# Kernel optimization log

Hardware: AMD Instinct MI355X
Metric: run time of the kernel (lower is better)

## Reference

```python
import jax, jax.numpy as jnp
import numpy as np

CLASH_WEIGHT = 0.05
PHYSICS_WEIGHT = 0.3
CLAMP_DIST = 10.0
EPS = 1e-8
C_IDX, N_IDX = 0, 1  # ATOM_TYPE_MAP['C'], ATOM_TYPE_MAP['N']


def setup_inputs() -> dict:
    key = jax.random.key(0)
    ks = jax.random.split(key, 8)
    B, R, A = 2, 1024, 4096
    return {
        'rots_pred': jax.random.normal(ks[0], (B, R, 3, 3), dtype=jnp.float32),
        'trans_pred': jax.random.normal(ks[1], (B, R, 3), dtype=jnp.float32),
        'coords_pred': jax.random.normal(ks[2], (B, A, 3), dtype=jnp.float32),
        'rots_true': jax.random.normal(ks[3], (B, R, 3, 3), dtype=jnp.float32),
        'trans_true': jax.random.normal(ks[4], (B, R, 3), dtype=jnp.float32),
        'coords_true': jax.random.normal(ks[5], (B, A, 3), dtype=jnp.float32),
        'atom_types': jax.random.randint(ks[6], (B, A), 0, 19, dtype=jnp.int32),
        'vdw_radii': jax.random.uniform(ks[7], (19,), dtype=jnp.float32),
        'res_mask': jnp.ones((B, R), dtype=jnp.float32),
        'mask': jnp.ones((B, A), dtype=jnp.float32),
    }


def _local_coords(rots, trans, coords):
    # invert_frames: R^-1 = R^T, t^-1 = -R^T t ; apply to all points per frame
    inv_rots = jnp.swapaxes(rots, -1, -2)                      # [B,R,3,3]
    inv_trans = -jnp.einsum('brij,brj->bri', inv_rots, trans)  # [B,R,3]
    # [B, R, A, 3]
    return jnp.einsum('brij,baj->brai', inv_rots, coords) + inv_trans[:, :, None, :]


def _pairwise_dist(coords, eps2=1e-12):
    # numerically-stable cdist via squared-norm expansion
    sq = jnp.sum(coords * coords, axis=-1)                      # [B,A]
    d2 = sq[:, :, None] + sq[:, None, :] - 2.0 * jnp.einsum('bad,bcd->bac', coords, coords)
    return jnp.sqrt(jnp.maximum(d2, eps2))                      # [B,A,A]


def reference(rots_pred, trans_pred, coords_pred, rots_true, trans_true,
              coords_true, atom_types, vdw_radii, res_mask, mask):
    # ---- FAPE ----
    lp = _local_coords(rots_pred, trans_pred, coords_pred)   # [B,R,A,3]
    lt = _local_coords(rots_true, trans_true, coords_true)   # [B,R,A,3]
    err = jnp.sqrt(jnp.sum((lp - lt) ** 2, axis=-1) + EPS)   # [B,R,A]
    err = jnp.minimum(err, CLAMP_DIST)
    err = err * mask[:, None, :] * res_mask[:, :, None]
    fape = jnp.sum(err) / (jnp.sum(mask) * jnp.sum(res_mask) + EPS)

    # shared pairwise distances on predicted coords
    d = _pairwise_dist(coords_pred)                          # [B,A,A]

    # ---- Clash ----
    radii = vdw_radii[atom_types]                            # [B,A]
    min_d = radii[:, :, None] + radii[:, None, :]
    clashes = (d < min_d) & (d > EPS)
    num_clashes = jnp.sum(clashes.astype(jnp.float32), axis=(-1, -2)) / 2.0
    num_atoms = coords_pred.shape[-2]
    clash = jnp.mean(num_clashes / num_atoms)

    # ---- Physics (C-N peptide bond length) ----
    is_c = atom_types == C_IDX
    is_n = atom_types == N_IDX
    cn_mask = (is_c[:, :, None] & is_n[:, None, :]).astype(jnp.float32)
    penalty = jax.nn.relu(jnp.abs(d - 1.33) - 0.2) * cn_mask
    total_pen = jnp.sum(penalty, axis=(-1, -2))
    n_pairs = jnp.maximum(jnp.sum(cn_mask, axis=(-1, -2)), 1.0)
    physics = jnp.mean(total_pen / n_pairs)

    total = fape + CLASH_WEIGHT * clash + PHYSICS_WEIGHT * physics
    return total
```

## Files before the change

kernel.cpp:

```cpp
#include <hip/hip_runtime.h>


constexpr int BB = 2;
constexpr int FR = 4;
constexpr int NI = 4;
constexpr int TJ = 16;
constexpr int IC = 1024;

constexpr int NB_FAPE = 512;
constexpr int NB_BAND = 512;
constexpr int NB_FULL = 768;
constexpr int NB_PAIR = NB_BAND + NB_FULL;

__device__ __forceinline__ float wred(float v) {
#pragma unroll
  for (int o = 32; o > 0; o >>= 1) v += __shfl_down(v, o, 64);
  return v;
}
__device__ __forceinline__ double wredd(double v) {
#pragma unroll
  for (int o = 32; o > 0; o >>= 1) v += __shfl_down(v, o, 64);
  return v;
}

template <bool BAND>
__device__ __forceinline__ void pair_body(
    const float* __restrict__ coords, const int* __restrict__ types,
    const float* __restrict__ vdw, int A, int b, int ic, int jt, int tid,
    float& out_clash, float& out_pen) {
  const int ibase = ic * IC;
  float xi[NI], yi[NI], zi[NI], qi[NI], ri[NI], cf[NI], nf[NI];
  int ii[NI];
#pragma unroll
  for (int k = 0; k < NI; ++k) {
    ii[k] = ibase + (k << 8) + tid;
    const size_t g = (size_t)b * A + ii[k];
    const float x = coords[g * 3], y = coords[g * 3 + 1], z = coords[g * 3 + 2];
    const int t = types[g];
    xi[k] = x; yi[k] = y; zi[k] = z;
    qi[k] = __fadd_rn(__fadd_rn(__fmul_rn(x, x), __fmul_rn(y, y)), __fmul_rn(z, z));
    ri[k] = vdw[t];
    cf[k] = (t == 0) ? 1.f : 0.f;
    nf[k] = (t == 1) ? 1.f : 0.f;
  }

  int cnt2 = 0, cnt1 = 0;
  float pen = 0.f;
  const int j0 = jt * TJ;
#pragma unroll 4
  for (int jj = 0; jj < TJ; ++jj) {
    const int j = j0 + jj;
    const size_t jg = (size_t)b * A + j;
    const float sx = coords[jg * 3], sy = coords[jg * 3 + 1], sz = coords[jg * 3 + 2];
    const int st = types[jg];
    const float sr = vdw[st];
    const float sq = __fadd_rn(__fadd_rn(__fmul_rn(sx, sx), __fmul_rn(sy, sy)),
                               __fmul_rn(sz, sz));
    float dsq[NI];
#pragma unroll
    for (int k = 0; k < NI; ++k) {
      const float dot = fmaf(zi[k], sz, fmaf(yi[k], sy, xi[k] * sx));
      float d2 = fmaf(-2.f, dot, qi[k] + sq);
      d2 = fmaxf(d2, 1e-12f);
      dsq[k] = d2;
      const float mind = ri[k] + sr;
      const bool c = d2 < mind * mind;
      if (BAND) {
        cnt2 += (c && (ii[k] < j)) ? 1 : 0;
        cnt1 += (c && (ii[k] == j)) ? 1 : 0;
      } else {
        cnt2 += c ? 1 : 0;
      }
    }
    if (st <= 1) {
      if (st == 1) {
#pragma unroll
        for (int k = 0; k < NI; ++k) {
          const float dd = __builtin_amdgcn_sqrtf(dsq[k]);
          float pp = fmaxf(fabsf(dd - 1.33f) - 0.2f, 0.f);
          if (BAND) pp = (ii[k] < j) ? pp : 0.f;
          pen = fmaf(pp, cf[k], pen);
        }
      } else {
#pragma unroll
        for (int k = 0; k < NI; ++k) {
          const float dd = __builtin_amdgcn_sqrtf(dsq[k]);
          float pp = fmaxf(fabsf(dd - 1.33f) - 0.2f, 0.f);
          if (BAND) pp = (ii[k] < j) ? pp : 0.f;
          pen = fmaf(pp, nf[k], pen);
        }
      }
    }
  }
  out_clash = 2.f * cnt2 + (float)cnt1;
  out_pen = pen;
}

__global__ __launch_bounds__(256) void fat_kernel(
    const float* __restrict__ rots_p, const float* __restrict__ trans_p,
    const float* __restrict__ coords_p,
    const float* __restrict__ rots_t, const float* __restrict__ trans_t,
    const float* __restrict__ coords_t,
    const int* __restrict__ types, const float* __restrict__ vdw,
    const float* __restrict__ res_mask, const float* __restrict__ mask,
    float* __restrict__ fape_part, float* __restrict__ clash_part,
    float* __restrict__ pen_part, int R, int A) {
  const int tid = threadIdx.x;
  const int bid = blockIdx.x;
  __shared__ float red[2][4];

  if (bid < NB_FAPE) {
    const int bpb = R / FR;
    const int b = bid / bpb;
    const int r0 = (bid % bpb) * FR;

    float rp[FR][9], rt[FR][9], cc[FR][3], rm[FR];
#pragma unroll
    for (int f = 0; f < FR; ++f) {
      const size_t fr = (size_t)(b * R + r0 + f);
      const float* Rp = rots_p + fr * 9;
      const float* Rt = rots_t + fr * 9;
      const float* Tp = trans_p + fr * 3;
      const float* Tt = trans_t + fr * 3;
#pragma unroll
      for (int k = 0; k < 9; ++k) { rp[f][k] = Rp[k]; rt[f][k] = Rt[k]; }
      const float tp0 = Tp[0], tp1 = Tp[1], tp2 = Tp[2];
      const float tt0 = Tt[0], tt1 = Tt[1], tt2 = Tt[2];
#pragma unroll
      for (int i = 0; i < 3; ++i) {
        cc[f][i] = (rp[f][0 + i] * tp0 + rp[f][3 + i] * tp1 + rp[f][6 + i] * tp2)
                 - (rt[f][0 + i] * tt0 + rt[f][3 + i] * tt1 + rt[f][6 + i] * tt2);
      }
      rm[f] = res_mask[fr];
    }

    float facc[FR];
#pragma unroll
    for (int f = 0; f < FR; ++f) facc[f] = 0.f;

    for (int a = tid; a < A; a += 256) {
      const size_t g = (size_t)b * A + a;
      const float x0 = coords_p[g * 3], x1 = coords_p[g * 3 + 1], x2 = coords_p[g * 3 + 2];
      const float y0 = coords_t[g * 3], y1 = coords_t[g * 3 + 1], y2 = coords_t[g * 3 + 2];
      const float m = mask[g];
#pragma unroll
      for (int f = 0; f < FR; ++f) {
        float u0 = fmaf(rp[f][0], x0, -cc[f][0]);
        u0 = fmaf(rp[f][3], x1, u0); u0 = fmaf(rp[f][6], x2, u0);
        u0 = fmaf(-rt[f][0], y0, u0); u0 = fmaf(-rt[f][3], y1, u0); u0 = fmaf(-rt[f][6], y2, u0);
        float u1 = fmaf(rp[f][1], x0, -cc[f][1]);
        u1 = fmaf(rp[f][4], x1, u1); u1 = fmaf(rp[f][7], x2, u1);
        u1 = fmaf(-rt[f][1], y0, u1); u1 = fmaf(-rt[f][4], y1, u1); u1 = fmaf(-rt[f][7], y2, u1);
        float u2 = fmaf(rp[f][2], x0, -cc[f][2]);
        u2 = fmaf(rp[f][5], x1, u2); u2 = fmaf(rp[f][8], x2, u2);
        u2 = fmaf(-rt[f][2], y0, u2); u2 = fmaf(-rt[f][5], y1, u2); u2 = fmaf(-rt[f][8], y2, u2);
        float e2 = fmaf(u0, u0, 1e-8f);
        e2 = fmaf(u1, u1, e2);
        e2 = fmaf(u2, u2, e2);
        float e = __builtin_amdgcn_sqrtf(e2);
        e = fminf(e, 10.0f);
        facc[f] = fmaf(e, m, facc[f]);
      }
    }

    float tot = 0.f;
#pragma unroll
    for (int f = 0; f < FR; ++f) tot = fmaf(facc[f], rm[f], tot);

    tot = wred(tot);
    if ((tid & 63) == 0) red[0][tid >> 6] = tot;
    __syncthreads();
    if (tid == 0) fape_part[bid] = red[0][0] + red[0][1] + red[0][2] + red[0][3];
    return;
  }

  int b, ic, jt;
  bool band;
  if (bid < NB_FAPE + NB_BAND) {
    const int q = bid - NB_FAPE;
    band = true;
    b = q >> 8;
    const int r = q & 255;
    ic = r >> 6;
    jt = (ic << 6) + (r & 63);
  } else {
    const int q = bid - (NB_FAPE + NB_BAND);
    band = false;
    b = q / 384;
    const int r = q % 384;
    if (r < 192)      { ic = 0; jt = 64 + r; }
    else if (r < 320) { ic = 1; jt = 128 + (r - 192); }
    else              { ic = 2; jt = 192 + (r - 320); }
  }

  float oc, op;
  if (band) pair_body<true >(coords_p, types, vdw, A, b, ic, jt, tid, oc, op);
  else      pair_body<false>(coords_p, types, vdw, A, b, ic, jt, tid, oc, op);

  const float rc = wred(oc);
  const float rpn = wred(op);
  if ((tid & 63) == 0) { red[0][tid >> 6] = rc; red[1][tid >> 6] = rpn; }
  __syncthreads();
  if (tid == 0) {
    const int pidx = bid - NB_FAPE;
    clash_part[pidx] = red[0][0] + red[0][1] + red[0][2] + red[0][3];
    pen_part[pidx]   = red[1][0] + red[1][1] + red[1][2] + red[1][3];
  }
}

__global__ __launch_bounds__(256) void finalize_kernel(
    const int* __restrict__ types, const float* __restrict__ res_mask,
    const float* __restrict__ mask,
    const float* __restrict__ fape_part, const float* __restrict__ clash_part,
    const float* __restrict__ pen_part,
    float* __restrict__ out, int R, int A) {
  const int tid = threadIdx.x;
  double sf = 0.0, sc0 = 0.0, sc1 = 0.0, sp0 = 0.0, sp1 = 0.0;
  for (int i = tid; i < NB_FAPE; i += 256) sf += (double)fape_part[i];
  for (int p = tid; p < NB_PAIR; p += 256) {
    const int bb = (p < NB_BAND) ? (p >> 8) : ((p - NB_BAND) / 384);
    const double c = (double)clash_part[p];
    const double pe = (double)pen_part[p];
    if (bb == 0) { sc0 += c; sp0 += pe; } else { sc1 += c; sp1 += pe; }
  }
  float cc0 = 0, cn0 = 0, cc1 = 0, cn1 = 0, sm = 0, srm = 0;
  for (int a = tid; a < A; a += 256) {
    const int t0 = types[a], t1 = types[A + a];
    cc0 += (t0 == 0) ? 1.f : 0.f;
    cn0 += (t0 == 1) ? 1.f : 0.f;
    cc1 += (t1 == 0) ? 1.f : 0.f;
    cn1 += (t1 == 1) ? 1.f : 0.f;
    sm += mask[a] + mask[A + a];
  }
  for (int r = tid; r < R; r += 256) srm += res_mask[r] + res_mask[R + r];

  __shared__ double dred[5][4];
  __shared__ float fred[6][4];
  double dv[5] = {sf, sc0, sc1, sp0, sp1};
  float fv[6] = {cc0, cn0, cc1, cn1, sm, srm};
#pragma unroll
  for (int k = 0; k < 5; ++k) {
    const double v = wredd(dv[k]);
    if ((tid & 63) == 0) dred[k][tid >> 6] = v;
  }
#pragma unroll
  for (int k = 0; k < 6; ++k) {
    const float v = wred(fv[k]);
    if ((tid & 63) == 0) fred[k][tid >> 6] = v;
  }
  __syncthreads();
  if (tid == 0) {
    double D[5];
    float F[6];
#pragma unroll
    for (int k = 0; k < 5; ++k) D[k] = dred[k][0] + dred[k][1] + dred[k][2] + dred[k][3];
#pragma unroll
    for (int k = 0; k < 6; ++k) F[k] = fred[k][0] + fred[k][1] + fred[k][2] + fred[k][3];
    const double fape = D[0] / ((double)F[4] * (double)F[5] + 1e-8);
    const double clash = (D[1] + D[2]) / (4.0 * (double)A);
    const double np0 = fmax((double)F[0] * (double)F[1], 1.0);
    const double np1 = fmax((double)F[2] * (double)F[3], 1.0);
    const double phys = 0.5 * (D[3] / np0 + D[4] / np1);
    out[0] = (float)(fape + 0.05 * clash + 0.3 * phys);
  }
}

extern "C" void kernel_launch(void* const* d_in, const int* in_sizes, int n_in,
                              void* d_out, int out_size, void* d_ws, size_t ws_size,
                              hipStream_t stream) {
  const float* rots_p   = (const float*)d_in[0];
  const float* trans_p  = (const float*)d_in[1];
  const float* coords_p = (const float*)d_in[2];
  const float* rots_t   = (const float*)d_in[3];
  const float* trans_t  = (const float*)d_in[4];
  const float* coords_t = (const float*)d_in[5];
  const int*   types    = (const int*)d_in[6];
  const float* vdw      = (const float*)d_in[7];
  const float* res_mask = (const float*)d_in[8];
  const float* mask     = (const float*)d_in[9];
  float* out = (float*)d_out;

  const int R = in_sizes[8] / BB;
  const int A = in_sizes[9] / BB;

  float* fape_part  = (float*)d_ws;
  float* clash_part = fape_part + NB_FAPE;
  float* pen_part   = clash_part + NB_PAIR;

  fat_kernel<<<NB_FAPE + NB_PAIR, 256, 0, stream>>>(
      rots_p, trans_p, coords_p, rots_t, trans_t, coords_t, types, vdw,
      res_mask, mask, fape_part, clash_part, pen_part, R, A);

  finalize_kernel<<<1, 256, 0, stream>>>(
      types, res_mask, mask, fape_part, clash_part, pen_part, out, R, A);
}
```

Before: 96.23 us.

## Interleave FAPE and pair blocks, halve frames per FAPE block, widen finalize

FAPE work is split across twice as many blocks with two frames each. FAPE and pairwise blocks are interleaved in a 4:5 pattern across the grid so the two workloads are spread over the CUs instead of running in separate phases. The finalize kernel moves to 1024 threads, and the penalty branch is merged into a single loop using a selected flag pointer. The cost is more blocks, each reloading its own frames and reducing separately, plus a larger cross-wave reduction in finalize.

```diff
diff --git a/kernel.cpp b/kernel.cpp
--- a/kernel.cpp
+++ b/kernel.cpp
@@ -2,15 +2,16 @@
 
 
 constexpr int BB = 2;
-constexpr int FR = 4;
+constexpr int FR = 2;
 constexpr int NI = 4;
 constexpr int TJ = 16;
 constexpr int IC = 1024;
 
-constexpr int NB_FAPE = 512;
+constexpr int NB_FAPE = 1024;
 constexpr int NB_BAND = 512;
 constexpr int NB_FULL = 768;
 constexpr int NB_PAIR = NB_BAND + NB_FULL;
+constexpr int NB_TOT = NB_FAPE + NB_PAIR;
 
 __device__ __forceinline__ float wred(float v) {
 #pragma unroll
@@ -73,22 +74,13 @@
       }
     }
     if (st <= 1) {
-      if (st == 1) {
-#pragma unroll
-        for (int k = 0; k < NI; ++k) {
-          const float dd = __builtin_amdgcn_sqrtf(dsq[k]);
-          float pp = fmaxf(fabsf(dd - 1.33f) - 0.2f, 0.f);
-          if (BAND) pp = (ii[k] < j) ? pp : 0.f;
-          pen = fmaf(pp, cf[k], pen);
-        }
-      } else {
-#pragma unroll
-        for (int k = 0; k < NI; ++k) {
-          const float dd = __builtin_amdgcn_sqrtf(dsq[k]);
-          float pp = fmaxf(fabsf(dd - 1.33f) - 0.2f, 0.f);
-          if (BAND) pp = (ii[k] < j) ? pp : 0.f;
-          pen = fmaf(pp, nf[k], pen);
-        }
+      const float* flag = (st == 1) ? cf : nf;
+#pragma unroll
+      for (int k = 0; k < NI; ++k) {
+        const float dd = __builtin_amdgcn_sqrtf(dsq[k]);
+        float pp = fmaxf(fabsf(dd - 1.33f) - 0.2f, 0.f);
+        if (BAND) pp = (ii[k] < j) ? pp : 0.f;
+        pen = fmaf(pp, flag[k], pen);
       }
     }
   }
@@ -107,12 +99,15 @@
     float* __restrict__ pen_part, int R, int A) {
   const int tid = threadIdx.x;
   const int bid = blockIdx.x;
+  const int g9 = bid / 9;
+  const int r9 = bid % 9;
   __shared__ float red[2][4];
 
-  if (bid < NB_FAPE) {
+  if (r9 < 4) {
+    const int fbid = g9 * 4 + r9;
     const int bpb = R / FR;
-    const int b = bid / bpb;
-    const int r0 = (bid % bpb) * FR;
+    const int b = fbid / bpb;
+    const int r0 = (fbid % bpb) * FR;
 
     float rp[FR][9], rt[FR][9], cc[FR][3], rm[FR];
 #pragma unroll
@@ -170,21 +165,21 @@
     tot = wred(tot);
     if ((tid & 63) == 0) red[0][tid >> 6] = tot;
     __syncthreads();
-    if (tid == 0) fape_part[bid] = red[0][0] + red[0][1] + red[0][2] + red[0][3];
+    if (tid == 0) fape_part[fbid] = red[0][0] + red[0][1] + red[0][2] + red[0][3];
     return;
   }
 
+  const int pbid = g9 * 5 + (r9 - 4);
   int b, ic, jt;
   bool band;
-  if (bid < NB_FAPE + NB_BAND) {
-    const int q = bid - NB_FAPE;
+  if (pbid < NB_BAND) {
     band = true;
-    b = q >> 8;
-    const int r = q & 255;
+    b = pbid >> 8;
+    const int r = pbid & 255;
     ic = r >> 6;
     jt = (ic << 6) + (r & 63);
   } else {
-    const int q = bid - (NB_FAPE + NB_BAND);
+    const int q = pbid - NB_BAND;
     band = false;
     b = q / 384;
     const int r = q % 384;
@@ -202,13 +197,12 @@
   if ((tid & 63) == 0) { red[0][tid >> 6] = rc; red[1][tid >> 6] = rpn; }
   __syncthreads();
   if (tid == 0) {
-    const int pidx = bid - NB_FAPE;
-    clash_part[pidx] = red[0][0] + red[0][1] + red[0][2] + red[0][3];
-    pen_part[pidx]   = red[1][0] + red[1][1] + red[1][2] + red[1][3];
-  }
-}
-
-__global__ __launch_bounds__(256) void finalize_kernel(
+    clash_part[pbid] = red[0][0] + red[0][1] + red[0][2] + red[0][3];
+    pen_part[pbid]   = red[1][0] + red[1][1] + red[1][2] + red[1][3];
+  }
+}
+
+__global__ __launch_bounds__(1024) void finalize_kernel(
     const int* __restrict__ types, const float* __restrict__ res_mask,
     const float* __restrict__ mask,
     const float* __restrict__ fape_part, const float* __restrict__ clash_part,
@@ -216,15 +210,15 @@
     float* __restrict__ out, int R, int A) {
   const int tid = threadIdx.x;
   double sf = 0.0, sc0 = 0.0, sc1 = 0.0, sp0 = 0.0, sp1 = 0.0;
-  for (int i = tid; i < NB_FAPE; i += 256) sf += (double)fape_part[i];
-  for (int p = tid; p < NB_PAIR; p += 256) {
+  for (int i = tid; i < NB_FAPE; i += 1024) sf += (double)fape_part[i];
+  for (int p = tid; p < NB_PAIR; p += 1024) {
     const int bb = (p < NB_BAND) ? (p >> 8) : ((p - NB_BAND) / 384);
     const double c = (double)clash_part[p];
     const double pe = (double)pen_part[p];
     if (bb == 0) { sc0 += c; sp0 += pe; } else { sc1 += c; sp1 += pe; }
   }
   float cc0 = 0, cn0 = 0, cc1 = 0, cn1 = 0, sm = 0, srm = 0;
-  for (int a = tid; a < A; a += 256) {
+  for (int a = tid; a < A; a += 1024) {
     const int t0 = types[a], t1 = types[A + a];
     cc0 += (t0 == 0) ? 1.f : 0.f;
     cn0 += (t0 == 1) ? 1.f : 0.f;
@@ -232,10 +226,10 @@
     cn1 += (t1 == 1) ? 1.f : 0.f;
     sm += mask[a] + mask[A + a];
   }
-  for (int r = tid; r < R; r += 256) srm += res_mask[r] + res_mask[R + r];
-
-  __shared__ double dred[5][4];
-  __shared__ float fred[6][4];
+  for (int r = tid; r < R; r += 1024) srm += res_mask[r] + res_mask[R + r];
+
+  __shared__ double dred[5][16];
+  __shared__ float fred[6][16];
   double dv[5] = {sf, sc0, sc1, sp0, sp1};
   float fv[6] = {cc0, cn0, cc1, cn1, sm, srm};
 #pragma unroll
@@ -253,9 +247,19 @@
     double D[5];
     float F[6];
 #pragma unroll
-    for (int k = 0; k < 5; ++k) D[k] = dred[k][0] + dred[k][1] + dred[k][2] + dred[k][3];
-#pragma unroll
-    for (int k = 0; k < 6; ++k) F[k] = fred[k][0] + fred[k][1] + fred[k][2] + fred[k][3];
+    for (int k = 0; k < 5; ++k) {
+      double s = 0.0;
+#pragma unroll
+      for (int w = 0; w < 16; ++w) s += dred[k][w];
+      D[k] = s;
+    }
+#pragma unroll
+    for (int k = 0; k < 6; ++k) {
+      float s = 0.f;
+#pragma unroll
+      for (int w = 0; w < 16; ++w) s += fred[k][w];
+      F[k] = s;
+    }
     const double fape = D[0] / ((double)F[4] * (double)F[5] + 1e-8);
     const double clash = (D[1] + D[2]) / (4.0 * (double)A);
     const double np0 = fmax((double)F[0] * (double)F[1], 1.0);
@@ -287,10 +291,10 @@
   float* clash_part = fape_part + NB_FAPE;
   float* pen_part   = clash_part + NB_PAIR;
 
-  fat_kernel<<<NB_FAPE + NB_PAIR, 256, 0, stream>>>(
+  fat_kernel<<<NB_TOT, 256, 0, stream>>>(
       rots_p, trans_p, coords_p, rots_t, trans_t, coords_t, types, vdw,
       res_mask, mask, fape_part, clash_part, pen_part, R, A);
 
-  finalize_kernel<<<1, 256, 0, stream>>>(
+  finalize_kernel<<<1, 1024, 0, stream>>>(
       types, res_mask, mask, fape_part, clash_part, pen_part, out, R, A);
 }
```

Result: no change. 95.14 us (-1.1%).
